# Performance work log

Hardware: AMD Instinct MI355X
Metric: run time of the kernel (lower is better)

The kernel has to match this reference:

```python
import jax, jax.numpy as jnp
import numpy as np
from jax import lax

N = 8192            # total ensemble boxes
W_IMG, H_IMG = 1920.0, 1080.0
NUM_MODELS = 5
CLUSTER_IOU = 0.5   # coalesce_boxes threshold


def setup_inputs() -> dict:
    key = jax.random.key(0)
    k1, k2, k3, k4, k5 = jax.random.split(key, 5)
    x1 = jax.random.uniform(k1, (N,)) * (W_IMG - 60.0)
    y1 = jax.random.uniform(k2, (N,)) * (H_IMG - 60.0)
    w = jax.random.uniform(k3, (N,)) * 180.0 + 4.0
    h = jax.random.uniform(k4, (N,)) * 180.0 + 4.0
    boxes = jnp.stack([x1, y1, x1 + w, y1 + h], axis=1)          # [N,4] xyxy
    scores = jax.random.uniform(k5, (N,)) * 0.7 + 0.3            # conf_thres=0.3
    return {"boxes": boxes, "scores": scores, "num_models": NUM_MODELS}


def _edf_forward(boxes, scores, num_models):
    n = boxes.shape[0]
    # clip to image (original also rounds; rounding omitted to keep grads alive)
    x1 = jnp.clip(boxes[:, 0], 0.0, W_IMG)
    y1 = jnp.clip(boxes[:, 1], 0.0, H_IMG)
    x2 = jnp.clip(boxes[:, 2], 0.0, W_IMG)
    y2 = jnp.clip(boxes[:, 3], 0.0, H_IMG)
    # coalesce_boxes processes boxes in descending score order (sort asc, pop)
    order = jnp.argsort(-scores)
    b = jnp.stack([x1, y1, x2, y2], axis=1)[order]               # [N,4]
    s = scores[order]
    bx1, by1, bx2, by2 = b[:, 0], b[:, 1], b[:, 2], b[:, 3]
    area = (bx2 - bx1 + 1.0) * (by2 - by1 + 1.0)
    # pairwise IoU with the +1 convention of bb_intersection_over_union
    ix1 = jnp.maximum(bx1[:, None], bx1[None, :])
    iy1 = jnp.maximum(by1[:, None], by1[None, :])
    ix2 = jnp.minimum(bx2[:, None], bx2[None, :])
    iy2 = jnp.minimum(by2[:, None], by2[None, :])
    inter = jnp.maximum(ix2 - ix1 + 1.0, 0.0) * jnp.maximum(iy2 - iy1 + 1.0, 0.0)
    iou = inter / (area[:, None] + area[None, :] - inter)        # [N,N]
    adj = iou > CLUSTER_IOU
    # greedy clustering: in score order, an unassigned box becomes a cluster
    # head and absorbs every still-unassigned box with IoU(head, j) > 0.5
    def step(cluster, i):
        is_head = cluster[i] < 0
        cluster = jnp.where(is_head & (cluster < 0) & adj[i], i, cluster)
        return cluster, None
    cluster, _ = lax.scan(step, jnp.full((n,), -1, jnp.int32),
                          jnp.arange(n, dtype=jnp.int32))
    counts = jax.ops.segment_sum(jnp.ones((n,), jnp.float32), cluster, num_segments=n)
    # per-group nms() only returns pick[0]: the member with max y2 (ties -> first)
    seg_y2 = jax.ops.segment_max(by2, cluster, num_segments=n)
    idx = jnp.arange(n)
    cand = by2 >= seg_y2[cluster]
    first = jax.ops.segment_min(jnp.where(cand, idx, n), cluster, num_segments=n)
    is_pick = idx == first[cluster]
    # probFinal = sum of group scores; final score = probFinal / num_models
    prob = jax.ops.segment_sum(s, cluster, num_segments=n)
    score_out = prob[cluster] / num_models
    # 'consensus': keep group iff its size >= num_models / 3
    valid = counts >= (num_models / 3.0)
    keep = is_pick & valid[cluster]
    out = jnp.where(keep[:, None],
                    jnp.concatenate([b, score_out[:, None]], axis=1),
                    0.0)                                         # [N,5] padded
    return out, keep


def reference(boxes, scores, num_models):
    return _edf_forward(boxes, scores, num_models)
```

## Files before the change

kernel.cpp:

```cpp
#include <hip/hip_runtime.h>
#include <cstdint>

#define N 8192
#define NT 128
#define NROUNDS 8
typedef unsigned long long u64;
typedef unsigned int u32;

__global__ __launch_bounds__(256) void k_init(const float* __restrict__ scores,
                                              u64* __restrict__ keys,
                                              int* __restrict__ rank,
                                              int* __restrict__ cnt,
                                              float* __restrict__ prob,
                                              unsigned* __restrict__ y2m,
                                              int* __restrict__ first,
                                              u64* __restrict__ D,
                                              u64* __restrict__ S) {
  int i = blockIdx.x * 256 + threadIdx.x;
  if (i >= N) return;
  float sc = scores[i];
  keys[i] = ((u64)__float_as_uint(sc) << 32) | (unsigned)(0xFFFFFFFFu - (unsigned)i);
  rank[i] = 0;
  cnt[i] = 0;
  prob[i] = 0.0f;
  y2m[i] = 0u;
  first[i] = N;
  if (i < NT) { D[i] = 0ull; S[i] = 0ull; }
}

__global__ __launch_bounds__(256) void k_rank(const u64* __restrict__ keys,
                                              int* __restrict__ rank) {
  __shared__ u64 tile[1024];
  int e = blockIdx.x * 256 + threadIdx.x;
  int j0 = blockIdx.y * 1024;
  for (int t = threadIdx.x; t < 1024; t += 256) tile[t] = keys[j0 + t];
  __syncthreads();
  u64 ke = keys[e];
  int c = 0;
#pragma unroll 8
  for (int k = 0; k < 1024; ++k) c += (tile[k] > ke) ? 1 : 0;
  atomicAdd(&rank[e], c);
}

__global__ __launch_bounds__(256) void k_scatter(const float* __restrict__ boxes,
                                                 const float* __restrict__ scores,
                                                 const int* __restrict__ rank,
                                                 float* __restrict__ bx1s, float* __restrict__ by1s,
                                                 float* __restrict__ bx2s, float* __restrict__ by2s,
                                                 float* __restrict__ ss, float* __restrict__ areas) {
#pragma clang fp contract(off)
  int i = blockIdx.x * 256 + threadIdx.x;
  if (i >= N) return;
  int r = rank[i];
  float x1 = fminf(fmaxf(boxes[i * 4 + 0], 0.0f), 1920.0f);
  float y1 = fminf(fmaxf(boxes[i * 4 + 1], 0.0f), 1080.0f);
  float x2 = fminf(fmaxf(boxes[i * 4 + 2], 0.0f), 1920.0f);
  float y2 = fminf(fmaxf(boxes[i * 4 + 3], 0.0f), 1080.0f);
  bx1s[r] = x1; by1s[r] = y1; bx2s[r] = x2; by2s[r] = y2;
  ss[r] = scores[i];
  areas[r] = (x2 - x1 + 1.0f) * (y2 - y1 + 1.0f);
}

__global__ __launch_bounds__(64) void k_adj(const float* __restrict__ bx1s, const float* __restrict__ by1s,
                                            const float* __restrict__ bx2s, const float* __restrict__ by2s,
                                            const float* __restrict__ areas,
                                            u64* __restrict__ mtile,
                                            u64* __restrict__ mrow) {
#pragma clang fp contract(off)
  __shared__ float jx1[64], jy1[64], jx2[64], jy2[64], ja[64];
  int p = blockIdx.x;
  int gy = (int)((sqrtf(8.0f * (float)p + 1.0f) - 1.0f) * 0.5f);
  while ((gy + 1) * (gy + 2) / 2 <= p) ++gy;
  while (gy * (gy + 1) / 2 > p) --gy;
  int gx = p - gy * (gy + 1) / 2;

  int l = threadIdx.x;
  int j = gx * 64 + l;
  jx1[l] = bx1s[j]; jy1[l] = by1s[j]; jx2[l] = bx2s[j]; jy2[l] = by2s[j]; ja[l] = areas[j];
  __syncthreads();
  int i = gy * 64 + l;
  float x1 = bx1s[i], y1 = by1s[i], x2 = bx2s[i], y2 = by2s[i], ai = areas[i];
  u64 bits = 0;
#pragma unroll 4
  for (int jj = 0; jj < 64; ++jj) {
    float ix1 = fmaxf(x1, jx1[jj]);
    float iy1 = fmaxf(y1, jy1[jj]);
    float ix2 = fminf(x2, jx2[jj]);
    float iy2 = fminf(y2, jy2[jj]);
    float iw = fmaxf(ix2 - ix1 + 1.0f, 0.0f);
    float ih = fmaxf(iy2 - iy1 + 1.0f, 0.0f);
    float inter = iw * ih;
    float uni = (ai + ja[jj]) - inter;
    float t = inter + inter;
    bool gt = t > uni;
    bool amb = fabsf(t - uni) <= 1e-6f * uni;
    if (__ballot(amb) != 0ull) {
      float iou = inter / uni;
      if (amb) gt = iou > 0.5f;
    }
    bits |= ((u64)gt) << jj;
  }
  mtile[((size_t)gy * NT + gx) * 64 + l] = bits;
  mrow[(size_t)i * NT + gx] = bits;
  if (gx != gy) {
    u64 tb = 0;
#pragma unroll 8
    for (int c = 0; c < 64; ++c) {
      u64 wb = __ballot((bits >> c) & 1ull);
      tb = (l == c) ? wb : tb;
    }
    mtile[((size_t)gx * NT + gy) * 64 + l] = tb;
    mrow[(size_t)(gx * 64 + l) * NT + gy] = tb;
  }
}

__global__ __launch_bounds__(256) void k_round(const u64* __restrict__ mtile,
                                               u64* __restrict__ D,
                                               u64* __restrict__ S) {
  __shared__ u64 Dl[NT], Sl[NT];
  __shared__ u64 bw[2][4];
  int gy = blockIdx.x;
  int t = threadIdx.x;
  if (t < NT) Dl[t] = D[t];
  else Sl[t - NT] = S[t - NT];
  __syncthreads();
  u64 classified = Dl[gy] | Sl[gy];
  if (classified == ~0ull) return;
  int w = t >> 6, r = t & 63;
  bool unk = !((classified >> r) & 1ull);
  u64 anyD = 0, anyU = 0;
  if (unk) {
    int k0 = 32 * w, k1 = min(k0 + 32, gy + 1);
    for (int k = k0; k < k1; ++k) {
      u64 m = mtile[((size_t)gy * NT + k) * 64 + r];
      if (k == gy) m &= (1ull << r) - 1ull;
      anyD |= (m & Dl[k]);
      anyU |= (m & ~Sl[k]);
    }
  }
  u64 bD = __ballot(anyD != 0ull), bU = __ballot(anyU != 0ull);
  if (r == 0) { bw[0][w] = bD; bw[1][w] = bU; }
  __syncthreads();
  if (t == 0) {
    u64 rD = bw[0][0] | bw[0][1] | bw[0][2] | bw[0][3];
    u64 rU = bw[1][0] | bw[1][1] | bw[1][2] | bw[1][3];
    u64 unkb = ~classified;
    u64 newS = unkb & rD;
    u64 newD = unkb & ~rD & ~rU;
    if (newS) atomicOr(&S[gy], newS);
    if (newD) atomicOr(&D[gy], newD);
  }
}

__global__ __launch_bounds__(64, 1) void k_fix(const u64* __restrict__ mrow,
                                               u64* __restrict__ D,
                                               const u64* __restrict__ S) {
  __shared__ int ulist[N];
  int l = threadIdx.x;
  u64 D0 = D[2 * l], D1 = D[2 * l + 1];
  u64 S0 = S[2 * l], S1 = S[2 * l + 1];
  u64 u0 = ~(D0 | S0), u1 = ~(D1 | S1);
  int cnt = __popcll(u0) + __popcll(u1);
  int pre = cnt;
  for (int d = 1; d < 64; d <<= 1) {
    int v = __shfl_up(pre, d);
    if (l >= d) pre += v;
  }
  int M = __shfl(pre, 63);
  int off = pre - cnt;
  {
    u64 v = u0; int o = off;
    while (v) { int b = __builtin_ctzll(v); v &= v - 1; ulist[o++] = l * 128 + b; }
    v = u1;
    while (v) { int b = __builtin_ctzll(v); v &= v - 1; ulist[o++] = l * 128 + 64 + b; }
  }
  __syncthreads();
  if (M > 0) {
    ulong2 ring[8];
    int pj[8];
#pragma unroll
    for (int q = 0; q < 8; ++q) {
      int j = ulist[q < M ? q : M - 1];
      pj[q] = j;
      ring[q] = *(const ulong2*)&mrow[(size_t)j * NT + 2 * l];
    }
    for (int m = 0; m < M; ++m) {
      int slot = m & 7;
      int j = pj[slot];
      ulong2 rv = ring[slot];
      int jt = j >> 6;
      u64 bm = (1ull << (j & 63)) - 1ull;
      u64 m0 = (2 * l < jt) ? ~0ull : ((2 * l == jt) ? bm : 0ull);
      u64 m1 = (2 * l + 1 < jt) ? ~0ull : ((2 * l + 1 == jt) ? bm : 0ull);
      bool hit = ((rv.x & D0 & m0) | (rv.y & D1 & m1)) != 0ull;
      bool head = (__ballot(hit) == 0ull);
      u64 bset = 1ull << (j & 63);
      D0 |= (head && (2 * l == jt)) ? bset : 0ull;
      D1 |= (head && (2 * l + 1 == jt)) ? bset : 0ull;
      int nm = m + 8;
      int j2 = ulist[nm < M ? nm : M - 1];
      pj[slot] = j2;
      ring[slot] = *(const ulong2*)&mrow[(size_t)j2 * NT + 2 * l];
    }
  }
  D[2 * l] = D0;
  D[2 * l + 1] = D1;
}

__global__ __launch_bounds__(256) void k_cluster(const u64* __restrict__ mtile,
                                                 const u64* __restrict__ D,
                                                 const float* __restrict__ ss,
                                                 const float* __restrict__ by2s,
                                                 int* __restrict__ cluster,
                                                 int* __restrict__ cnt,
                                                 float* __restrict__ prob,
                                                 unsigned* __restrict__ y2m) {
  __shared__ u64 hlds[NT];
  __shared__ int red[4][64];
  int gy = blockIdx.x;
  if (threadIdx.x < NT) hlds[threadIdx.x] = D[threadIdx.x];
  __syncthreads();
  int w = threadIdx.x >> 6, r = threadIdx.x & 63;
  int best = 0x7fffffff;
  for (int kk = 0; kk < 32; ++kk) {
    int k = 32 * w + kk;
    u64 v = mtile[((size_t)gy * NT + k) * 64 + r] & hlds[k];
    if (v && best == 0x7fffffff) best = k * 64 + __builtin_ctzll(v);
  }
  red[w][r] = best;
  __syncthreads();
  if (w == 0) {
    int b = min(min(red[0][r], red[1][r]), min(red[2][r], red[3][r]));
    int j = gy * 64 + r;
    cluster[j] = b;
    atomicAdd(&cnt[b], 1);
    atomicAdd(&prob[b], ss[j]);
    atomicMax(&y2m[b], __float_as_uint(by2s[j]));
  }
}

__global__ __launch_bounds__(256) void k_first(const int* __restrict__ cluster,
                                               const float* __restrict__ by2s,
                                               const unsigned* __restrict__ y2m,
                                               int* __restrict__ first) {
  int j = blockIdx.x * 256 + threadIdx.x;
  if (j >= N) return;
  int c = cluster[j];
  if (by2s[j] >= __uint_as_float(y2m[c])) atomicMin(&first[c], j);
}

__global__ __launch_bounds__(256) void k_out(const int* __restrict__ cluster,
                                             const float* __restrict__ bx1s, const float* __restrict__ by1s,
                                             const float* __restrict__ bx2s, const float* __restrict__ by2s,
                                             const int* __restrict__ cnt,
                                             const float* __restrict__ prob,
                                             const int* __restrict__ first,
                                             const int* __restrict__ num_models,
                                             float* __restrict__ out) {
  int j = blockIdx.x * 256 + threadIdx.x;
  if (j >= N) return;
  int c = cluster[j];
  int nm = num_models[0];
  bool valid = (float)cnt[c] >= (float)nm / 3.0f;
  bool pick = (first[c] == j);
  bool keep = pick && valid;
  float o0 = 0.f, o1 = 0.f, o2 = 0.f, o3 = 0.f, o4 = 0.f;
  if (keep) {
    o0 = bx1s[j]; o1 = by1s[j]; o2 = bx2s[j]; o3 = by2s[j];
    o4 = prob[c] / (float)nm;
  }
  out[j * 5 + 0] = o0;
  out[j * 5 + 1] = o1;
  out[j * 5 + 2] = o2;
  out[j * 5 + 3] = o3;
  out[j * 5 + 4] = o4;
  out[N * 5 + j] = keep ? 1.0f : 0.0f;
}

extern "C" void kernel_launch(void* const* d_in, const int* in_sizes, int n_in,
                              void* d_out, int out_size, void* d_ws, size_t ws_size,
                              hipStream_t stream) {
  const float* boxes = (const float*)d_in[0];
  const float* scores = (const float*)d_in[1];
  const int* num_models = (const int*)d_in[2];
  float* out = (float*)d_out;

  char* p = (char*)d_ws;
  auto take = [&](size_t bytes) {
    char* r = p;
    p += (bytes + 255) & ~(size_t)255;
    return r;
  };
  u64* keys   = (u64*)take((size_t)N * 8);
  int* rank   = (int*)take((size_t)N * 4);
  float* bx1s = (float*)take((size_t)N * 4);
  float* by1s = (float*)take((size_t)N * 4);
  float* bx2s = (float*)take((size_t)N * 4);
  float* by2s = (float*)take((size_t)N * 4);
  float* ss   = (float*)take((size_t)N * 4);
  float* areas= (float*)take((size_t)N * 4);
  int* cluster= (int*)take((size_t)N * 4);
  int* cnt    = (int*)take((size_t)N * 4);
  float* prob = (float*)take((size_t)N * 4);
  unsigned* y2m = (unsigned*)take((size_t)N * 4);
  int* first  = (int*)take((size_t)N * 4);
  u64* D      = (u64*)take((size_t)NT * 8);
  u64* S      = (u64*)take((size_t)NT * 8);
  u64* mtile  = (u64*)take((size_t)NT * NT * 64 * 8);
  u64* mrow   = (u64*)take((size_t)N * NT * 8);

  k_init<<<N / 256, 256, 0, stream>>>(scores, keys, rank, cnt, prob, y2m, first, D, S);
  k_rank<<<dim3(N / 256, 8), 256, 0, stream>>>(keys, rank);
  k_scatter<<<N / 256, 256, 0, stream>>>(boxes, scores, rank, bx1s, by1s, bx2s, by2s, ss, areas);
  k_adj<<<NT * (NT + 1) / 2, 64, 0, stream>>>(bx1s, by1s, bx2s, by2s, areas, mtile, mrow);
  for (int r = 0; r < NROUNDS; ++r)
    k_round<<<NT, 256, 0, stream>>>(mtile, D, S);
  k_fix<<<1, 64, 0, stream>>>(mrow, D, S);
  k_cluster<<<N / 64, 256, 0, stream>>>(mtile, D, ss, by2s, cluster, cnt, prob, y2m);
  k_first<<<N / 256, 256, 0, stream>>>(cluster, by2s, y2m, first);
  k_out<<<N / 256, 256, 0, stream>>>(cluster, bx1s, by1s, bx2s, by2s, cnt, prob, first, num_models, out);
}
```

Before: 177.6 us.

## Merge head-resolution rounds into one persistent kernel with in-tile greedy finish

Replaces eight separate round launches with one kernel whose blocks iterate up to twelve times. Each iteration re-reads the D/S bitmasks through relaxed atomic loads, so blocks can see progress made by other blocks within the same launch. When a tile has no unresolved dependencies on earlier tiles, one wave finishes the greedy head selection inside the diagonal tile, using readlane over the tile's rows, and exits early. The adjacency kernel now packs four tile pairs per 256-thread block to cut block count and launch overhead. The risk is that correctness and the number of iterations depend on how cross-block progress becomes visible, which leans more heavily on the k_fix fallback.

```diff
diff --git a/kernel.cpp b/kernel.cpp
--- a/kernel.cpp
+++ b/kernel.cpp
@@ -3,9 +3,15 @@
 
 #define N 8192
 #define NT 128
-#define NROUNDS 8
+#define RITERS 12
 typedef unsigned long long u64;
 typedef unsigned int u32;
+
+__device__ inline u64 readlane64(u64 v, int lane) {
+  u32 lo = (u32)__builtin_amdgcn_readlane((int)(u32)v, lane);
+  u32 hi = (u32)__builtin_amdgcn_readlane((int)(u32)(v >> 32), lane);
+  return ((u64)hi << 32) | lo;
+}
 
 __global__ __launch_bounds__(256) void k_init(const float* __restrict__ scores,
                                               u64* __restrict__ keys,
@@ -61,36 +67,36 @@
   areas[r] = (x2 - x1 + 1.0f) * (y2 - y1 + 1.0f);
 }
 
-__global__ __launch_bounds__(64) void k_adj(const float* __restrict__ bx1s, const float* __restrict__ by1s,
-                                            const float* __restrict__ bx2s, const float* __restrict__ by2s,
-                                            const float* __restrict__ areas,
-                                            u64* __restrict__ mtile,
-                                            u64* __restrict__ mrow) {
+__global__ __launch_bounds__(256) void k_adj(const float* __restrict__ bx1s, const float* __restrict__ by1s,
+                                             const float* __restrict__ bx2s, const float* __restrict__ by2s,
+                                             const float* __restrict__ areas,
+                                             u64* __restrict__ mtile,
+                                             u64* __restrict__ mrow) {
 #pragma clang fp contract(off)
-  __shared__ float jx1[64], jy1[64], jx2[64], jy2[64], ja[64];
-  int p = blockIdx.x;
+  __shared__ float jx1[4][64], jy1[4][64], jx2[4][64], jy2[4][64], ja[4][64];
+  int w = threadIdx.x >> 6, l = threadIdx.x & 63;
+  int p = blockIdx.x * 4 + w;
   int gy = (int)((sqrtf(8.0f * (float)p + 1.0f) - 1.0f) * 0.5f);
   while ((gy + 1) * (gy + 2) / 2 <= p) ++gy;
   while (gy * (gy + 1) / 2 > p) --gy;
   int gx = p - gy * (gy + 1) / 2;
 
-  int l = threadIdx.x;
   int j = gx * 64 + l;
-  jx1[l] = bx1s[j]; jy1[l] = by1s[j]; jx2[l] = bx2s[j]; jy2[l] = by2s[j]; ja[l] = areas[j];
+  jx1[w][l] = bx1s[j]; jy1[w][l] = by1s[j]; jx2[w][l] = bx2s[j]; jy2[w][l] = by2s[j]; ja[w][l] = areas[j];
   __syncthreads();
   int i = gy * 64 + l;
   float x1 = bx1s[i], y1 = by1s[i], x2 = bx2s[i], y2 = by2s[i], ai = areas[i];
   u64 bits = 0;
 #pragma unroll 4
   for (int jj = 0; jj < 64; ++jj) {
-    float ix1 = fmaxf(x1, jx1[jj]);
-    float iy1 = fmaxf(y1, jy1[jj]);
-    float ix2 = fminf(x2, jx2[jj]);
-    float iy2 = fminf(y2, jy2[jj]);
+    float ix1 = fmaxf(x1, jx1[w][jj]);
+    float iy1 = fmaxf(y1, jy1[w][jj]);
+    float ix2 = fminf(x2, jx2[w][jj]);
+    float iy2 = fminf(y2, jy2[w][jj]);
     float iw = fmaxf(ix2 - ix1 + 1.0f, 0.0f);
     float ih = fmaxf(iy2 - iy1 + 1.0f, 0.0f);
     float inter = iw * ih;
-    float uni = (ai + ja[jj]) - inter;
+    float uni = (ai + ja[w][jj]) - inter;
     float t = inter + inter;
     bool gt = t > uni;
     bool amb = fabsf(t - uni) <= 1e-6f * uni;
@@ -114,41 +120,75 @@
   }
 }
 
-__global__ __launch_bounds__(256) void k_round(const u64* __restrict__ mtile,
-                                               u64* __restrict__ D,
-                                               u64* __restrict__ S) {
+__global__ __launch_bounds__(256) void k_rounds(const u64* __restrict__ mtile,
+                                                u64* __restrict__ D,
+                                                u64* __restrict__ S) {
   __shared__ u64 Dl[NT], Sl[NT];
-  __shared__ u64 bw[2][4];
+  __shared__ u64 bw[3][4];
+  __shared__ u64 fD, fU, fE;
   int gy = blockIdx.x;
   int t = threadIdx.x;
-  if (t < NT) Dl[t] = D[t];
-  else Sl[t - NT] = S[t - NT];
-  __syncthreads();
-  u64 classified = Dl[gy] | Sl[gy];
-  if (classified == ~0ull) return;
   int w = t >> 6, r = t & 63;
-  bool unk = !((classified >> r) & 1ull);
-  u64 anyD = 0, anyU = 0;
-  if (unk) {
-    int k0 = 32 * w, k1 = min(k0 + 32, gy + 1);
-    for (int k = k0; k < k1; ++k) {
-      u64 m = mtile[((size_t)gy * NT + k) * 64 + r];
-      if (k == gy) m &= (1ull << r) - 1ull;
-      anyD |= (m & Dl[k]);
-      anyU |= (m & ~Sl[k]);
-    }
-  }
-  u64 bD = __ballot(anyD != 0ull), bU = __ballot(anyU != 0ull);
-  if (r == 0) { bw[0][w] = bD; bw[1][w] = bU; }
-  __syncthreads();
-  if (t == 0) {
-    u64 rD = bw[0][0] | bw[0][1] | bw[0][2] | bw[0][3];
-    u64 rU = bw[1][0] | bw[1][1] | bw[1][2] | bw[1][3];
+  u64 dAA = (w == 0) ? mtile[((size_t)gy * NT + gy) * 64 + r] : 0ull;
+
+  for (int it = 0; it < RITERS; ++it) {
+    if (t < NT) Dl[t] = __hip_atomic_load(&D[t], __ATOMIC_RELAXED, __HIP_MEMORY_SCOPE_AGENT);
+    else Sl[t - NT] = __hip_atomic_load(&S[t - NT], __ATOMIC_RELAXED, __HIP_MEMORY_SCOPE_AGENT);
+    __syncthreads();
+    u64 classified = Dl[gy] | Sl[gy];
+    if (classified == ~0ull) return;
+    bool unk = !((classified >> r) & 1ull);
+    u64 anyD = 0, anyU = 0, anyE = 0;
+    if (unk) {
+      int k0 = 32 * w, k1 = min(k0 + 32, gy + 1);
+      for (int k = k0; k < k1; ++k) {
+        u64 m = mtile[((size_t)gy * NT + k) * 64 + r];
+        if (k == gy) {
+          m &= (1ull << r) - 1ull;
+          anyD |= m & Dl[k];
+          anyU |= m & ~Sl[k];
+        } else {
+          anyD |= m & Dl[k];
+          anyU |= m & ~Sl[k];
+          anyE |= m & ~(Sl[k] | Dl[k]);
+        }
+      }
+    }
+    u64 bD = __ballot(anyD != 0ull), bU = __ballot(anyU != 0ull), bE = __ballot(anyE != 0ull);
+    if (r == 0) { bw[0][w] = bD; bw[1][w] = bU; bw[2][w] = bE; }
+    __syncthreads();
+    if (t == 0) {
+      fD = bw[0][0] | bw[0][1] | bw[0][2] | bw[0][3];
+      fU = bw[1][0] | bw[1][1] | bw[1][2] | bw[1][3];
+      fE = bw[2][0] | bw[2][1] | bw[2][2] | bw[2][3];
+    }
+    __syncthreads();
+    u64 rD = fD, rU = fU, rE = fE;
     u64 unkb = ~classified;
-    u64 newS = unkb & rD;
-    u64 newD = unkb & ~rD & ~rU;
-    if (newS) atomicOr(&S[gy], newS);
-    if (newD) atomicOr(&D[gy], newD);
+    if (rE == 0ull) {
+      if (w == 0) {
+        u64 t0 = unkb & ~rD;
+        u64 heads = 0, todo = t0;
+        while (todo) {
+          int i = __builtin_ctzll(todo);
+          heads |= 1ull << i;
+          todo &= ~readlane64(dAA, i);
+        }
+        if (r == 0) {
+          if (heads) atomicOr(&D[gy], heads);
+          u64 ns = unkb & ~heads;
+          if (ns) atomicOr(&S[gy], ns);
+        }
+      }
+      return;
+    }
+    if (t == 0) {
+      u64 newS = unkb & rD;
+      u64 newD = unkb & ~rD & ~rU;
+      if (newS) atomicOr(&S[gy], newS);
+      if (newD) atomicOr(&D[gy], newD);
+    }
+    __syncthreads();
   }
 }
 
@@ -312,9 +352,8 @@
   k_init<<<N / 256, 256, 0, stream>>>(scores, keys, rank, cnt, prob, y2m, first, D, S);
   k_rank<<<dim3(N / 256, 8), 256, 0, stream>>>(keys, rank);
   k_scatter<<<N / 256, 256, 0, stream>>>(boxes, scores, rank, bx1s, by1s, bx2s, by2s, ss, areas);
-  k_adj<<<NT * (NT + 1) / 2, 64, 0, stream>>>(bx1s, by1s, bx2s, by2s, areas, mtile, mrow);
-  for (int r = 0; r < NROUNDS; ++r)
-    k_round<<<NT, 256, 0, stream>>>(mtile, D, S);
+  k_adj<<<NT * (NT + 1) / 2 / 4, 256, 0, stream>>>(bx1s, by1s, bx2s, by2s, areas, mtile, mrow);
+  k_rounds<<<NT, 256, 0, stream>>>(mtile, D, S);
   k_fix<<<1, 64, 0, stream>>>(mrow, D, S);
   k_cluster<<<N / 64, 256, 0, stream>>>(mtile, D, ss, by2s, cluster, cnt, prob, y2m);
   k_first<<<N / 256, 256, 0, stream>>>(cluster, by2s, y2m, first);
```

New measurement: 179.6 us. Within noise of the previous version (+1.1%).
